# Kernel tuning notes

Hardware: AMD Instinct MI355X
Metric: run time of the kernel (lower is better)

## Reference

```python
import jax, jax.numpy as jnp
import numpy as np

B, C, H, T, K = 8, 256, 256, 4096, 2  # batch, input_size, hidden_size, seq_len, kernel_size


def setup_inputs() -> dict:
    key = jax.random.key(0)
    ks = jax.random.split(key, 9)
    x = jax.random.normal(ks[0], (B, C, T), dtype=jnp.float32)
    w = lambda k: jax.random.normal(k, (H, C, K), dtype=jnp.float32) * 0.05
    b = lambda k: jax.random.normal(k, (H,), dtype=jnp.float32) * 0.05
    return {
        "x": x,
        "Wz": w(ks[1]), "bz": b(ks[2]),
        "Wf": w(ks[3]), "bf": b(ks[4]),
        "Wo": w(ks[5]), "bo": b(ks[6]),
        "Wi": w(ks[7]), "bi": b(ks[8]),
    }


def _causal_conv(x, W, b):
    # x: [B, C, T], W: [H, C, K]; left-pad by K-1 zeros == torch.cat([zeros, x]) then valid conv
    k = W.shape[-1]
    y = jax.lax.conv_general_dilated(
        x, W, window_strides=(1,), padding=[(k - 1, 0)],
        dimension_numbers=("NCH", "OIH", "NCH"))
    return y + b[None, :, None]


def reference(x, Wz, bz, Wf, bf, Wo, bo, Wi, bi):
    z = jnp.tanh(_causal_conv(x, Wz, bz))          # [B, H, T]
    f = jax.nn.sigmoid(_causal_conv(x, Wf, bf))    # zoneout=0 -> plain sigmoid
    o = jax.nn.sigmoid(_causal_conv(x, Wo, bo))
    i = jax.nn.sigmoid(_causal_conv(x, Wi, bi))    # computed as in original; unused for 'fo' pooling
    del i

    # fo-pooling recurrence: c_t = f_t * c_{t-1} + (1 - f_t) * z_t ; h_t = o_t * c_t
    f_tbh = jnp.transpose(f, (2, 0, 1))  # [T, B, H]
    z_tbh = jnp.transpose(z, (2, 0, 1))
    c0 = jnp.zeros((x.shape[0], Wz.shape[0]), dtype=x.dtype)

    def step(c_prev, fz):
        f_t, z_t = fz
        c_t = f_t * c_prev + (1.0 - f_t) * z_t
        return c_t, c_t

    _, cs = jax.lax.scan(step, c0, (f_tbh, z_tbh))  # [T, B, H]
    c = jnp.transpose(cs, (1, 2, 0))                # [B, H, T]
    h = o * c
    return (h, c)
```

## Files before the change

kernel.cpp:

```cpp
#include <hip/hip_runtime.h>


typedef unsigned short ushort_t;
typedef __attribute__((ext_vector_type(8))) short short8_t;
typedef __attribute__((ext_vector_type(4))) float f32x4;

#define B_ 8
#define C_ 256
#define H_ 256
#define T_ 4096
#define TCH 32
#define NCH 128

__device__ __forceinline__ unsigned short f2bf(float f) {
  unsigned int u = __float_as_uint(f);
  u += 0x7fffu + ((u >> 16) & 1u);
  return (unsigned short)(u >> 16);
}
__device__ __forceinline__ float bf2f(unsigned short u) {
  return __uint_as_float(((unsigned int)u) << 16);
}
__device__ __forceinline__ float sigm(float v) { return 1.f / (1.f + __expf(-v)); }
__device__ __forceinline__ float tanh_f(float v) { return 2.f / (1.f + __expf(-2.f * v)) - 1.f; }

__device__ __forceinline__ void gl16(const ushort_t* g, ushort_t* l) {
  __builtin_amdgcn_global_load_lds(
      (const __attribute__((address_space(1))) unsigned int*)g,
      (__attribute__((address_space(3))) unsigned int*)l, 16, 0, 0);
}

__global__ __launch_bounds__(256) void qrnn_pack_x(const float* __restrict__ x,
                                                   ushort_t* __restrict__ xq) {
  __shared__ float tile[32][132];
  const int tid = threadIdx.x;
  const int t0 = blockIdx.x * 128, c0 = blockIdx.y * 32, b = blockIdx.z;
#pragma unroll
  for (int p = 0; p < 5; ++p) {
    const int idx = tid + p * 256;
    if (idx < 1056) {
      const int row = idx / 33, q = idx % 33;
      const int tg = t0 - 4 + q * 4;
      float4 v = make_float4(0.f, 0.f, 0.f, 0.f);
      if (tg >= 0)
        v = *reinterpret_cast<const float4*>(x + ((size_t)(b * C_ + c0 + row)) * T_ + tg);
      tile[row][q * 4 + 0] = v.x; tile[row][q * 4 + 1] = v.y;
      tile[row][q * 4 + 2] = v.z; tile[row][q * 4 + 3] = v.w;
    }
  }
  __syncthreads();
  const int ks0 = c0 >> 5;
#pragma unroll
  for (int q2 = 0; q2 < 2; ++q2) {
    const int p = tid + q2 * 256;
    const int tfl = p >> 6, lane = p & 63;
    const int l15 = lane & 15, g8 = (lane >> 4) * 8;
    const int tcol = tfl * 16 + l15;
    ushort_t o0[8], o1[8];
#pragma unroll
    for (int j = 0; j < 8; ++j) {
      o0[j] = f2bf(tile[g8 + j][tcol + 4]);
      o1[j] = f2bf(tile[g8 + j][tcol + 3]);
    }
    const int tf = (t0 >> 4) + tfl;
    ushort_t* d0 = xq + ((size_t)((b * 256 + tf) * 16 + ks0) * 64 + lane) * 8;
    ushort_t* d1 = xq + ((size_t)((b * 256 + tf) * 16 + 8 + ks0) * 64 + lane) * 8;
    *reinterpret_cast<uint4*>(d0) = *reinterpret_cast<uint4*>(&o0[0]);
    *reinterpret_cast<uint4*>(d1) = *reinterpret_cast<uint4*>(&o1[0]);
  }
}

__global__ __launch_bounds__(256) void qrnn_pack_w(const float* __restrict__ Wz,
                                                   const float* __restrict__ Wf,
                                                   const float* __restrict__ Wo,
                                                   ushort_t* __restrict__ aq) {
  const int idx = blockIdx.x * 256 + threadIdx.x;
  const int lane = idx & 63;
  const int ks = (idx >> 6) & 15;
  const int mf = idx >> 10;
  const int hs = mf / 12, rem = mf % 12;
  const int g = rem >> 2, hlf = rem & 3;
  const int h = hs * 64 + hlf * 16 + (lane & 15);
  const float* W = (g == 0) ? Wz : ((g == 1) ? Wf : Wo);
  ushort_t o[8];
#pragma unroll
  for (int j = 0; j < 8; ++j) {
    const int k = ks * 32 + (lane >> 4) * 8 + j;
    const int c = k & 255;
    const int tap = (k < 256) ? 1 : 0;
    o[j] = f2bf(W[((size_t)h * C_ + c) * 2 + tap]);
  }
  *reinterpret_cast<uint4*>(aq + (size_t)idx * 8) = *reinterpret_cast<uint4*>(&o[0]);
}

__global__ __launch_bounds__(512, 4) void qrnn_g(const ushort_t* __restrict__ aq,
                                                 const ushort_t* __restrict__ xq,
                                                 const float* __restrict__ bz,
                                                 const float* __restrict__ bfv,
                                                 const float* __restrict__ bo,
                                                 float* __restrict__ fb,
                                                 ushort_t* __restrict__ zb,
                                                 ushort_t* __restrict__ ob) {
  __shared__ ushort_t As[12 * 2 * 64 * 8];
  __shared__ ushort_t Bs[8 * 2 * 64 * 8];
  const int tid = threadIdx.x;
  const int lane = tid & 63;
  const int wid = tid >> 6;
  const int wm = wid >> 1, wt = wid & 1;
  const int l15 = lane & 15, g4 = lane >> 4;
  const int tt = blockIdx.x;
  const int hs = blockIdx.y;
  const int b = blockIdx.z;

  f32x4 acc[3][4];
#pragma unroll
  for (int i = 0; i < 3; ++i)
#pragma unroll
    for (int n = 0; n < 4; ++n) acc[i][n] = (f32x4){0.f, 0.f, 0.f, 0.f};

  const int cA0 = tid, cA1 = tid + 512, cA2 = tid + 1024;
  const int wbase = tid - lane;

  for (int kk = 0; kk < 8; ++kk) {
    {
      const int c = cA0;
      gl16(aq + ((size_t)((hs * 12 + (c >> 7)) * 16 + kk * 2 + ((c >> 6) & 1)) << 9) + lane * 8,
           As + (size_t)(c - lane) * 8);
    }
    {
      const int c = cA1;
      gl16(aq + ((size_t)((hs * 12 + (c >> 7)) * 16 + kk * 2 + ((c >> 6) & 1)) << 9) + lane * 8,
           As + (size_t)(c - lane) * 8);
    }
    {
      const int c = cA2;
      gl16(aq + ((size_t)((hs * 12 + (c >> 7)) * 16 + kk * 2 + ((c >> 6) & 1)) << 9) + lane * 8,
           As + (size_t)(c - lane) * 8);
    }
#pragma unroll
    for (int q = 0; q < 2; ++q) {
      const int c2 = tid + q * 512;
      gl16(xq + ((size_t)((b * 256 + tt * 8 + (c2 >> 7)) * 16 + kk * 2 + ((c2 >> 6) & 1)) << 9) +
               lane * 8,
           Bs + (size_t)(c2 - lane) * 8);
    }
    __syncthreads();

#pragma unroll
    for (int l = 0; l < 2; ++l) {
      short8_t a[3], bb[4];
#pragma unroll
      for (int i = 0; i < 3; ++i)
        a[i] = *reinterpret_cast<const short8_t*>(
            &As[(size_t)((((wm * 3 + i) * 2 + l) * 64) + lane) * 8]);
#pragma unroll
      for (int n = 0; n < 4; ++n)
        bb[n] = *reinterpret_cast<const short8_t*>(
            &Bs[(size_t)((((wt * 4 + n) * 2 + l) * 64) + lane) * 8]);
#pragma unroll
      for (int i = 0; i < 3; ++i)
#pragma unroll
        for (int n = 0; n < 4; ++n)
          acc[i][n] = __builtin_amdgcn_mfma_f32_16x16x32_bf16(a[i], bb[n], acc[i][n], 0, 0, 0);
    }
    __syncthreads();
  }

#pragma unroll
  for (int i = 0; i < 3; ++i) {
    const int mfl = wm * 3 + i;
    const int g = mfl >> 2;
    const int hl0 = (mfl & 3) * 16;
    const float* bias = (g == 0) ? bz : ((g == 1) ? bfv : bo);
#pragma unroll
    for (int r = 0; r < 4; ++r) {
      const int h = hs * 64 + hl0 + g4 * 4 + r;
      const float bvv = bias[h];
      const size_t rowoff = ((size_t)b * H_ + h) * T_;
#pragma unroll
      for (int n = 0; n < 4; ++n) {
        const int t = tt * 128 + wt * 64 + n * 16 + l15;
        const float v = acc[i][n][r] + bvv;
        if (g == 0)      zb[rowoff + t] = f2bf(tanh_f(v));
        else if (g == 1) fb[rowoff + t] = sigm(v);
        else             ob[rowoff + t] = f2bf(sigm(v));
      }
    }
  }
}

__global__ __launch_bounds__(256) void qrnn_s1(const float* __restrict__ fb,
                                               const ushort_t* __restrict__ zb,
                                               float* __restrict__ aggP,
                                               float* __restrict__ aggC) {
  __shared__ float lf[256][33];
  __shared__ ushort_t lzs[256][36];
  const int tid = threadIdx.x;
  const int chunk = blockIdx.x;
  const int b = blockIdx.y;
  const int t0 = chunk * TCH;
  const float* fbase = fb + (size_t)b * H_ * T_;
  const ushort_t* zbase = zb + (size_t)b * H_ * T_;
  const int lr = tid >> 3, lc = (tid & 7) * 4;
#pragma unroll
  for (int pass = 0; pass < 8; ++pass) {
    const int row = pass * 32 + lr;
    float4 fv = *reinterpret_cast<const float4*>(fbase + (size_t)row * T_ + t0 + lc);
    uint2 zv = *reinterpret_cast<const uint2*>(zbase + (size_t)row * T_ + t0 + lc);
    lf[row][lc] = fv.x; lf[row][lc + 1] = fv.y; lf[row][lc + 2] = fv.z; lf[row][lc + 3] = fv.w;
    lzs[row][lc] = (ushort_t)(zv.x & 0xffff); lzs[row][lc + 1] = (ushort_t)(zv.x >> 16);
    lzs[row][lc + 2] = (ushort_t)(zv.y & 0xffff); lzs[row][lc + 3] = (ushort_t)(zv.y >> 16);
  }
  __syncthreads();
  float c = 0.f, p = 1.f;
#pragma unroll
  for (int t = 0; t < TCH; ++t) {
    const float f = lf[tid][t], z = bf2f(lzs[tid][t]);
    c = f * (c - z) + z;
    p *= f;
  }
  aggP[((size_t)b * NCH + chunk) * H_ + tid] = p;
  aggC[((size_t)b * NCH + chunk) * H_ + tid] = c;
}

__global__ __launch_bounds__(256) void qrnn_s2(const float* __restrict__ aggP,
                                               const float* __restrict__ aggC,
                                               float* __restrict__ cin) {
  const int b = blockIdx.x, h = threadIdx.x;
  float carry = 0.f;
  for (int jb = 0; jb < NCH; jb += 8) {
    float P[8], Cv[8];
#pragma unroll
    for (int u = 0; u < 8; ++u) {
      P[u] = aggP[((size_t)b * NCH + jb + u) * H_ + h];
      Cv[u] = aggC[((size_t)b * NCH + jb + u) * H_ + h];
    }
#pragma unroll
    for (int u = 0; u < 8; ++u) {
      cin[((size_t)b * NCH + jb + u) * H_ + h] = carry;
      carry = Cv[u] + P[u] * carry;
    }
  }
}

__global__ __launch_bounds__(256) void qrnn_s3(const float* __restrict__ fb,
                                               const ushort_t* __restrict__ zb,
                                               const ushort_t* __restrict__ ob,
                                               const float* __restrict__ cin,
                                               float* __restrict__ outc,
                                               float* __restrict__ outh) {
  __shared__ float lf[128][33];
  __shared__ ushort_t lzs[128][36];
  __shared__ ushort_t los[128][36];
  const int tid = threadIdx.x;
  const int chunk = blockIdx.x;
  const int h0 = blockIdx.y * 128;
  const int b = blockIdx.z;
  const int t0 = chunk * TCH;
  const float* fbase = fb + (size_t)b * H_ * T_;
  const ushort_t* zbase = zb + (size_t)b * H_ * T_;
  const ushort_t* obase = ob + (size_t)b * H_ * T_;
#pragma unroll
  for (int i = 0; i < 4; ++i) {
    const int j = tid + i * 256;
    const int row = j >> 3, c4 = (j & 7) * 4;
    const size_t goff = (size_t)(h0 + row) * T_ + t0 + c4;
    float4 fv = *reinterpret_cast<const float4*>(fbase + goff);
    uint2 zv = *reinterpret_cast<const uint2*>(zbase + goff);
    uint2 ov = *reinterpret_cast<const uint2*>(obase + goff);
    lf[row][c4] = fv.x; lf[row][c4 + 1] = fv.y; lf[row][c4 + 2] = fv.z; lf[row][c4 + 3] = fv.w;
    lzs[row][c4] = (ushort_t)(zv.x & 0xffff); lzs[row][c4 + 1] = (ushort_t)(zv.x >> 16);
    lzs[row][c4 + 2] = (ushort_t)(zv.y & 0xffff); lzs[row][c4 + 3] = (ushort_t)(zv.y >> 16);
    los[row][c4] = (ushort_t)(ov.x & 0xffff); los[row][c4 + 1] = (ushort_t)(ov.x >> 16);
    los[row][c4 + 2] = (ushort_t)(ov.y & 0xffff); los[row][c4 + 3] = (ushort_t)(ov.y >> 16);
  }
  __syncthreads();
  if (tid < 128) {
    float c = cin[((size_t)b * NCH + chunk) * H_ + h0 + tid];
#pragma unroll
    for (int t = 0; t < TCH; ++t) {
      const float f = lf[tid][t], z = bf2f(lzs[tid][t]);
      c = f * (c - z) + z;
      lf[tid][t] = c;
    }
  }
  __syncthreads();
  float* cb = outc + (size_t)b * H_ * T_;
  float* hb = outh + (size_t)b * H_ * T_;
#pragma unroll
  for (int i = 0; i < 4; ++i) {
    const int j = tid + i * 256;
    const int row = j >> 3, c4 = (j & 7) * 4;
    const size_t goff = (size_t)(h0 + row) * T_ + t0 + c4;
    float4 cv = make_float4(lf[row][c4], lf[row][c4 + 1], lf[row][c4 + 2], lf[row][c4 + 3]);
    float4 hv = make_float4(bf2f(los[row][c4]) * cv.x, bf2f(los[row][c4 + 1]) * cv.y,
                            bf2f(los[row][c4 + 2]) * cv.z, bf2f(los[row][c4 + 3]) * cv.w);
    *reinterpret_cast<float4*>(cb + goff) = cv;
    *reinterpret_cast<float4*>(hb + goff) = hv;
  }
}

extern "C" void kernel_launch(void* const* d_in, const int* in_sizes, int n_in,
                              void* d_out, int out_size, void* d_ws, size_t ws_size,
                              hipStream_t stream) {
  const float* x  = (const float*)d_in[0];
  const float* Wz = (const float*)d_in[1];
  const float* bz = (const float*)d_in[2];
  const float* Wf = (const float*)d_in[3];
  const float* bfv= (const float*)d_in[4];
  const float* Wo = (const float*)d_in[5];
  const float* bo = (const float*)d_in[6];

  float* outh = (float*)d_out;
  float* outc = outh + (size_t)B_ * H_ * T_;

  constexpr size_t XQ_OFF  = 0;
  constexpr size_t AQ_OFF  = 33554432;
  constexpr size_t FB_OFF  = 34340864;
  constexpr size_t ZB_OFF  = 67895296;
  constexpr size_t OB_OFF  = 84672512;
  constexpr size_t AGP_OFF = 101449728;
  constexpr size_t AGC_OFF = 102498304;
  constexpr size_t CIN_OFF = 103546880;
  constexpr size_t WS_NEED = 104595456;
  if (ws_size < WS_NEED) return;

  ushort_t* xq = (ushort_t*)((char*)d_ws + XQ_OFF);
  ushort_t* aq = (ushort_t*)((char*)d_ws + AQ_OFF);
  float* fbuf  = (float*)((char*)d_ws + FB_OFF);
  ushort_t* zb = (ushort_t*)((char*)d_ws + ZB_OFF);
  ushort_t* ob = (ushort_t*)((char*)d_ws + OB_OFF);
  float* aggP  = (float*)((char*)d_ws + AGP_OFF);
  float* aggC  = (float*)((char*)d_ws + AGC_OFF);
  float* cin   = (float*)((char*)d_ws + CIN_OFF);

  qrnn_pack_x<<<dim3(T_ / 128, C_ / 32, B_), 256, 0, stream>>>(x, xq);
  qrnn_pack_w<<<dim3(192), 256, 0, stream>>>(Wz, Wf, Wo, aq);
  qrnn_g<<<dim3(T_ / 128, 4, B_), 512, 0, stream>>>(aq, xq, bz, bfv, bo, fbuf, zb, ob);
  qrnn_s1<<<dim3(NCH, B_), 256, 0, stream>>>(fbuf, zb, aggP, aggC);
  qrnn_s2<<<dim3(B_), 256, 0, stream>>>(aggP, aggC, cin);
  qrnn_s3<<<dim3(NCH, 2, B_), 256, 0, stream>>>(fbuf, zb, ob, cin, outc, outh);
}
```

Baseline: 110.5 us.

## Fuse chunk-local scan into GEMM epilogue and simplify final carry pass

The GEMM kernel now stages tanh(z) and sigmoid(f) tiles in LDS, runs the per-chunk local scan there, and writes the local cell state plus the cumulative f-product (bf16), along with the chunk aggregates. This removes the separate s1 pass that re-read f and z from global memory. The final pass becomes a flat elementwise kernel, c = c_local + P*carry and h = o*c, with no per-thread serial loop. The trade-offs are a larger LDS footprint (about 66KB per block, which may cut occupancy under launch_bounds 512,4), a bf16-rounded prefix product, and a flattened grid order.

```diff
diff --git a/kernel.cpp b/kernel.cpp
--- a/kernel.cpp
+++ b/kernel.cpp
@@ -11,6 +11,7 @@
 #define T_ 4096
 #define TCH 32
 #define NCH 128
+#define LZP 129
 
 __device__ __forceinline__ unsigned short f2bf(float f) {
   unsigned int u = __float_as_uint(f);
@@ -97,19 +98,26 @@
                                                  const float* __restrict__ bz,
                                                  const float* __restrict__ bfv,
                                                  const float* __restrict__ bo,
-                                                 float* __restrict__ fb,
-                                                 ushort_t* __restrict__ zb,
-                                                 ushort_t* __restrict__ ob) {
-  __shared__ ushort_t As[12 * 2 * 64 * 8];
-  __shared__ ushort_t Bs[8 * 2 * 64 * 8];
+                                                 float* __restrict__ cl,
+                                                 ushort_t* __restrict__ pb,
+                                                 ushort_t* __restrict__ ob,
+                                                 float* __restrict__ aggP,
+                                                 float* __restrict__ aggC) {
+  __shared__ __align__(16) char ldsu[66048];
+  ushort_t* As = (ushort_t*)ldsu;
+  ushort_t* Bs = (ushort_t*)(ldsu + 24576);
+  float* lz = (float*)ldsu;
+  float* lf = (float*)(ldsu + 33024);
+
   const int tid = threadIdx.x;
   const int lane = tid & 63;
   const int wid = tid >> 6;
   const int wm = wid >> 1, wt = wid & 1;
   const int l15 = lane & 15, g4 = lane >> 4;
-  const int tt = blockIdx.x;
-  const int hs = blockIdx.y;
-  const int b = blockIdx.z;
+  const int bid = blockIdx.x;
+  const int b = bid & 7;
+  const int hs = (bid >> 3) & 3;
+  const int tt = bid >> 5;
 
   f32x4 acc[3][4];
 #pragma unroll
@@ -117,22 +125,10 @@
 #pragma unroll
     for (int n = 0; n < 4; ++n) acc[i][n] = (f32x4){0.f, 0.f, 0.f, 0.f};
 
-  const int cA0 = tid, cA1 = tid + 512, cA2 = tid + 1024;
-  const int wbase = tid - lane;
-
   for (int kk = 0; kk < 8; ++kk) {
-    {
-      const int c = cA0;
-      gl16(aq + ((size_t)((hs * 12 + (c >> 7)) * 16 + kk * 2 + ((c >> 6) & 1)) << 9) + lane * 8,
-           As + (size_t)(c - lane) * 8);
-    }
-    {
-      const int c = cA1;
-      gl16(aq + ((size_t)((hs * 12 + (c >> 7)) * 16 + kk * 2 + ((c >> 6) & 1)) << 9) + lane * 8,
-           As + (size_t)(c - lane) * 8);
-    }
-    {
-      const int c = cA2;
+#pragma unroll
+    for (int q = 0; q < 3; ++q) {
+      const int c = tid + q * 512;
       gl16(aq + ((size_t)((hs * 12 + (c >> 7)) * 16 + kk * 2 + ((c >> 6) & 1)) << 9) + lane * 8,
            As + (size_t)(c - lane) * 8);
     }
@@ -144,7 +140,6 @@
            Bs + (size_t)(c2 - lane) * 8);
     }
     __syncthreads();
-
 #pragma unroll
     for (int l = 0; l < 2; ++l) {
       short8_t a[3], bb[4];
@@ -173,53 +168,58 @@
     const float* bias = (g == 0) ? bz : ((g == 1) ? bfv : bo);
 #pragma unroll
     for (int r = 0; r < 4; ++r) {
-      const int h = hs * 64 + hl0 + g4 * 4 + r;
-      const float bvv = bias[h];
-      const size_t rowoff = ((size_t)b * H_ + h) * T_;
+      const int hl = hl0 + g4 * 4 + r;
+      const float bvv = bias[hs * 64 + hl];
 #pragma unroll
       for (int n = 0; n < 4; ++n) {
-        const int t = tt * 128 + wt * 64 + n * 16 + l15;
+        const int tl = wt * 64 + n * 16 + l15;
         const float v = acc[i][n][r] + bvv;
-        if (g == 0)      zb[rowoff + t] = f2bf(tanh_f(v));
-        else if (g == 1) fb[rowoff + t] = sigm(v);
-        else             ob[rowoff + t] = f2bf(sigm(v));
+        if (g == 0)      lz[hl * LZP + tl] = tanh_f(v);
+        else if (g == 1) lf[hl * LZP + tl] = sigm(v);
+        else ob[((size_t)b * H_ + hs * 64 + hl) * T_ + tt * 128 + tl] = f2bf(sigm(v));
       }
     }
   }
-}
-
-__global__ __launch_bounds__(256) void qrnn_s1(const float* __restrict__ fb,
-                                               const ushort_t* __restrict__ zb,
-                                               float* __restrict__ aggP,
-                                               float* __restrict__ aggC) {
-  __shared__ float lf[256][33];
-  __shared__ ushort_t lzs[256][36];
-  const int tid = threadIdx.x;
-  const int chunk = blockIdx.x;
-  const int b = blockIdx.y;
-  const int t0 = chunk * TCH;
-  const float* fbase = fb + (size_t)b * H_ * T_;
-  const ushort_t* zbase = zb + (size_t)b * H_ * T_;
-  const int lr = tid >> 3, lc = (tid & 7) * 4;
-#pragma unroll
-  for (int pass = 0; pass < 8; ++pass) {
-    const int row = pass * 32 + lr;
-    float4 fv = *reinterpret_cast<const float4*>(fbase + (size_t)row * T_ + t0 + lc);
-    uint2 zv = *reinterpret_cast<const uint2*>(zbase + (size_t)row * T_ + t0 + lc);
-    lf[row][lc] = fv.x; lf[row][lc + 1] = fv.y; lf[row][lc + 2] = fv.z; lf[row][lc + 3] = fv.w;
-    lzs[row][lc] = (ushort_t)(zv.x & 0xffff); lzs[row][lc + 1] = (ushort_t)(zv.x >> 16);
-    lzs[row][lc + 2] = (ushort_t)(zv.y & 0xffff); lzs[row][lc + 3] = (ushort_t)(zv.y >> 16);
-  }
   __syncthreads();
-  float c = 0.f, p = 1.f;
-#pragma unroll
-  for (int t = 0; t < TCH; ++t) {
-    const float f = lf[tid][t], z = bf2f(lzs[tid][t]);
-    c = f * (c - z) + z;
-    p *= f;
-  }
-  aggP[((size_t)b * NCH + chunk) * H_ + tid] = p;
-  aggC[((size_t)b * NCH + chunk) * H_ + tid] = c;
+
+  if (tid < 256) {
+    const int h = tid & 63, ch = tid >> 6;
+    float* pz = lz + h * LZP + ch * 32;
+    float* pf = lf + h * LZP + ch * 32;
+    float c = 0.f, p = 1.f;
+#pragma unroll
+    for (int t = 0; t < TCH; ++t) {
+      const float f = pf[t], z = pz[t];
+      c = f * (c - z) + z;
+      p *= f;
+      pz[t] = c;
+      pf[t] = p;
+    }
+    const int chunkg = tt * 4 + ch;
+    aggP[((size_t)b * NCH + chunkg) * H_ + hs * 64 + h] = p;
+    aggC[((size_t)b * NCH + chunkg) * H_ + hs * 64 + h] = c;
+  }
+  __syncthreads();
+
+  float* clb = cl + ((size_t)b * H_ + hs * 64) * T_ + tt * 128;
+#pragma unroll
+  for (int q = 0; q < 4; ++q) {
+    const int j = tid + q * 512;
+    const int row = j >> 5, col = (j & 31) * 4;
+    float4 v = make_float4(lz[row * LZP + col], lz[row * LZP + col + 1],
+                           lz[row * LZP + col + 2], lz[row * LZP + col + 3]);
+    *reinterpret_cast<float4*>(clb + (size_t)row * T_ + col) = v;
+  }
+  ushort_t* pbb = pb + ((size_t)b * H_ + hs * 64) * T_ + tt * 128;
+#pragma unroll
+  for (int q = 0; q < 2; ++q) {
+    const int j = tid + q * 512;
+    const int row = j >> 4, col = (j & 15) * 8;
+    ushort_t o8[8];
+#pragma unroll
+    for (int k = 0; k < 8; ++k) o8[k] = f2bf(lf[row * LZP + col + k]);
+    *reinterpret_cast<uint4*>(pbb + (size_t)row * T_ + col) = *reinterpret_cast<uint4*>(&o8[0]);
+  }
 }
 
 __global__ __launch_bounds__(256) void qrnn_s2(const float* __restrict__ aggP,
@@ -242,60 +242,32 @@
   }
 }
 
-__global__ __launch_bounds__(256) void qrnn_s3(const float* __restrict__ fb,
-                                               const ushort_t* __restrict__ zb,
+__global__ __launch_bounds__(256) void qrnn_s3(const float* __restrict__ cl,
+                                               const ushort_t* __restrict__ pb,
                                                const ushort_t* __restrict__ ob,
                                                const float* __restrict__ cin,
                                                float* __restrict__ outc,
                                                float* __restrict__ outh) {
-  __shared__ float lf[128][33];
-  __shared__ ushort_t lzs[128][36];
-  __shared__ ushort_t los[128][36];
-  const int tid = threadIdx.x;
-  const int chunk = blockIdx.x;
-  const int h0 = blockIdx.y * 128;
-  const int b = blockIdx.z;
-  const int t0 = chunk * TCH;
-  const float* fbase = fb + (size_t)b * H_ * T_;
-  const ushort_t* zbase = zb + (size_t)b * H_ * T_;
-  const ushort_t* obase = ob + (size_t)b * H_ * T_;
-#pragma unroll
-  for (int i = 0; i < 4; ++i) {
-    const int j = tid + i * 256;
-    const int row = j >> 3, c4 = (j & 7) * 4;
-    const size_t goff = (size_t)(h0 + row) * T_ + t0 + c4;
-    float4 fv = *reinterpret_cast<const float4*>(fbase + goff);
-    uint2 zv = *reinterpret_cast<const uint2*>(zbase + goff);
-    uint2 ov = *reinterpret_cast<const uint2*>(obase + goff);
-    lf[row][c4] = fv.x; lf[row][c4 + 1] = fv.y; lf[row][c4 + 2] = fv.z; lf[row][c4 + 3] = fv.w;
-    lzs[row][c4] = (ushort_t)(zv.x & 0xffff); lzs[row][c4 + 1] = (ushort_t)(zv.x >> 16);
-    lzs[row][c4 + 2] = (ushort_t)(zv.y & 0xffff); lzs[row][c4 + 3] = (ushort_t)(zv.y >> 16);
-    los[row][c4] = (ushort_t)(ov.x & 0xffff); los[row][c4 + 1] = (ushort_t)(ov.x >> 16);
-    los[row][c4 + 2] = (ushort_t)(ov.y & 0xffff); los[row][c4 + 3] = (ushort_t)(ov.y >> 16);
-  }
-  __syncthreads();
-  if (tid < 128) {
-    float c = cin[((size_t)b * NCH + chunk) * H_ + h0 + tid];
-#pragma unroll
-    for (int t = 0; t < TCH; ++t) {
-      const float f = lf[tid][t], z = bf2f(lzs[tid][t]);
-      c = f * (c - z) + z;
-      lf[tid][t] = c;
-    }
-  }
-  __syncthreads();
-  float* cb = outc + (size_t)b * H_ * T_;
-  float* hb = outh + (size_t)b * H_ * T_;
-#pragma unroll
-  for (int i = 0; i < 4; ++i) {
-    const int j = tid + i * 256;
-    const int row = j >> 3, c4 = (j & 7) * 4;
-    const size_t goff = (size_t)(h0 + row) * T_ + t0 + c4;
-    float4 cv = make_float4(lf[row][c4], lf[row][c4 + 1], lf[row][c4 + 2], lf[row][c4 + 3]);
-    float4 hv = make_float4(bf2f(los[row][c4]) * cv.x, bf2f(los[row][c4 + 1]) * cv.y,
-                            bf2f(los[row][c4 + 2]) * cv.z, bf2f(los[row][c4 + 3]) * cv.w);
-    *reinterpret_cast<float4*>(cb + goff) = cv;
-    *reinterpret_cast<float4*>(hb + goff) = hv;
+  const int n4 = B_ * H_ * T_ / 4;
+  for (int i4 = blockIdx.x * 256 + threadIdx.x; i4 < n4; i4 += gridDim.x * 256) {
+    const int idx = i4 << 2;
+    const int t = idx & (T_ - 1);
+    const int bh = idx >> 12;
+    const float carry = cin[((size_t)(bh >> 8) * NCH + (t >> 5)) * H_ + (bh & 255)];
+    float4 clv = reinterpret_cast<const float4*>(cl)[i4];
+    uint2 pv = reinterpret_cast<const uint2*>(pb)[i4];
+    uint2 ov = reinterpret_cast<const uint2*>(ob)[i4];
+    const float c0 = clv.x + bf2f((ushort_t)(pv.x & 0xffff)) * carry;
+    const float c1 = clv.y + bf2f((ushort_t)(pv.x >> 16)) * carry;
+    const float c2 = clv.z + bf2f((ushort_t)(pv.y & 0xffff)) * carry;
+    const float c3 = clv.w + bf2f((ushort_t)(pv.y >> 16)) * carry;
+    float4 cv = make_float4(c0, c1, c2, c3);
+    float4 hv = make_float4(bf2f((ushort_t)(ov.x & 0xffff)) * c0,
+                            bf2f((ushort_t)(ov.x >> 16)) * c1,
+                            bf2f((ushort_t)(ov.y & 0xffff)) * c2,
+                            bf2f((ushort_t)(ov.y >> 16)) * c3);
+    reinterpret_cast<float4*>(outc)[i4] = cv;
+    reinterpret_cast<float4*>(outh)[i4] = hv;
   }
 }
 
@@ -315,8 +287,8 @@
 
   constexpr size_t XQ_OFF  = 0;
   constexpr size_t AQ_OFF  = 33554432;
-  constexpr size_t FB_OFF  = 34340864;
-  constexpr size_t ZB_OFF  = 67895296;
+  constexpr size_t CL_OFF  = 34340864;
+  constexpr size_t PB_OFF  = 67895296;
   constexpr size_t OB_OFF  = 84672512;
   constexpr size_t AGP_OFF = 101449728;
   constexpr size_t AGC_OFF = 102498304;
@@ -326,8 +298,8 @@
 
   ushort_t* xq = (ushort_t*)((char*)d_ws + XQ_OFF);
   ushort_t* aq = (ushort_t*)((char*)d_ws + AQ_OFF);
-  float* fbuf  = (float*)((char*)d_ws + FB_OFF);
-  ushort_t* zb = (ushort_t*)((char*)d_ws + ZB_OFF);
+  float* clb   = (float*)((char*)d_ws + CL_OFF);
+  ushort_t* pbb= (ushort_t*)((char*)d_ws + PB_OFF);
   ushort_t* ob = (ushort_t*)((char*)d_ws + OB_OFF);
   float* aggP  = (float*)((char*)d_ws + AGP_OFF);
   float* aggC  = (float*)((char*)d_ws + AGC_OFF);
@@ -335,8 +307,7 @@
 
   qrnn_pack_x<<<dim3(T_ / 128, C_ / 32, B_), 256, 0, stream>>>(x, xq);
   qrnn_pack_w<<<dim3(192), 256, 0, stream>>>(Wz, Wf, Wo, aq);
-  qrnn_g<<<dim3(T_ / 128, 4, B_), 512, 0, stream>>>(aq, xq, bz, bfv, bo, fbuf, zb, ob);
-  qrnn_s1<<<dim3(NCH, B_), 256, 0, stream>>>(fbuf, zb, aggP, aggC);
+  qrnn_g<<<dim3(1024), 512, 0, stream>>>(aq, xq, bz, bfv, bo, clb, pbb, ob, aggP, aggC);
   qrnn_s2<<<dim3(B_), 256, 0, stream>>>(aggP, aggC, cin);
-  qrnn_s3<<<dim3(NCH, 2, B_), 256, 0, stream>>>(fbuf, zb, ob, cin, outc, outh);
-}
+  qrnn_s3<<<dim3(2048), 256, 0, stream>>>(clb, pbb, ob, cin, outc, outh);
+}
```

After: 100.1 us. 9.4% less time.
